# Kernel optimization log

Hardware: AMD Instinct MI355X
Metric: run time of the kernel (lower is better)

## Reference

```python
import jax, jax.numpy as jnp
import numpy as np

DIM = 1024
HEADS = 16
EPS = 1e-5  # torch nn.LayerNorm default
SCALE = (DIM / HEADS) ** -0.5


def _layernorm(x, w, b):
    mu = jnp.mean(x, axis=-1, keepdims=True)
    var = jnp.mean((x - mu) ** 2, axis=-1, keepdims=True)
    return (x - mu) * jax.lax.rsqrt(var + EPS) * w + b


def setup_inputs() -> dict:
    key = jax.random.key(0)
    ks = jax.random.split(key, 12)
    B, Lq, Lk, C, g = 2, 1024, 2048, DIM, HEADS
    c = C // g
    inp = {
        "q": jax.random.normal(ks[0], (B, Lq, C), jnp.float32),
        "k": jax.random.normal(ks[1], (B, Lk, C), jnp.float32),
        "v": jax.random.normal(ks[2], (B, Lk, C), jnp.float32),
        "qpos": jax.random.normal(ks[3], (B, Lq, g, c), jnp.float32),
        "kpos": jax.random.normal(ks[4], (B, Lk, g, c), jnp.float32),
        "mask": jax.random.randint(ks[5], (B, 1, 1, Lk), 0, 2, jnp.int32),
        # LayerNorm params
        "ln_q_w": jnp.ones((C,), jnp.float32),
        "ln_q_b": jnp.zeros((C,), jnp.float32),
        "ln_k_w": jnp.ones((C,), jnp.float32),
        "ln_k_b": jnp.zeros((C,), jnp.float32),
        "ln_v_w": jnp.ones((C,), jnp.float32),
        "ln_v_b": jnp.zeros((C,), jnp.float32),
        # Linear weights, torch layout [out, in]; qkv_bias=False
        "w_q": jax.random.normal(ks[6], (C, C), jnp.float32) * 0.02,
        "w_k": jax.random.normal(ks[7], (C, C), jnp.float32) * 0.02,
        "w_v": jax.random.normal(ks[8], (C, C), jnp.float32) * 0.02,
        "w_proj": jax.random.normal(ks[9], (C, C), jnp.float32) * 0.02,
        "b_proj": jnp.zeros((C,), jnp.float32),
    }
    return inp


def reference(q, k, v, qpos, kpos, mask,
              ln_q_w, ln_q_b, ln_k_w, ln_k_b, ln_v_w, ln_v_b,
              w_q, w_k, w_v, w_proj, b_proj):
    B, Lq, C = q.shape
    g = HEADS
    c = C // g
    Lk = k.shape[1]

    # apply_pos: pos is [B, N, g, c]; add per-head then flatten back
    q = (q.reshape(B, Lq, g, c) + qpos).reshape(B, Lq, C)
    k = (k.reshape(B, Lk, g, c) + kpos).reshape(B, Lk, C)

    qn = _layernorm(q, ln_q_w, ln_q_b)
    kn = _layernorm(k, ln_k_w, ln_k_b)
    vn = _layernorm(v, ln_v_w, ln_v_b)

    # torch Linear: x @ W.T
    q4 = jnp.einsum('bnc,dc->bnd', qn, w_q).reshape(B, Lq, g, c)
    k4 = jnp.einsum('bnc,dc->bnd', kn, w_k).reshape(B, Lk, g, c)
    v4 = jnp.einsum('bnc,dc->bnd', vn, w_v).reshape(B, Lk, g, c)

    # scores: [B, q, g, k] (note head dim is axis 2, matching original einsum)
    attn = jnp.einsum('bqgc,bkgc->bqgk', q4, k4) * SCALE
    m = mask.astype(bool)  # [B,1,1,Lk] broadcasts over q and g
    attn = jnp.where(m, -jnp.inf, attn)
    p = jax.nn.softmax(attn, axis=-1)
    p = jnp.where(m, 0.0, p)

    out = jnp.einsum('bqgk,bkgc->bqgc', p, v4).reshape(B, Lq, C)
    out = jnp.einsum('bnc,dc->bnd', out, w_proj) + b_proj
    return out
```

## Files before the change

kernel.cpp:

```cpp
#include <hip/hip_runtime.h>
#include <stdint.h>
#include <stddef.h>

typedef __bf16 bf16;
typedef bf16 bf16x2 __attribute__((ext_vector_type(2)));
typedef bf16 bf16x4 __attribute__((ext_vector_type(4)));
typedef bf16 bf16x8 __attribute__((ext_vector_type(8)));
typedef float f32x4 __attribute__((ext_vector_type(4)));
typedef float f32x16 __attribute__((ext_vector_type(16)));

#define MFMA16(a, b, c) __builtin_amdgcn_mfma_f32_16x16x32_bf16((a), (b), (c), 0, 0, 0)
#define MFMA32(a, b, c) __builtin_amdgcn_mfma_f32_32x32x16_bf16((a), (b), (c), 0, 0, 0)

#define GLD_LDS16(g, l)                                          \
    __builtin_amdgcn_global_load_lds(                            \
        (const __attribute__((address_space(1))) void*)(g),      \
        (__attribute__((address_space(3))) void*)(l), 16, 0, 0)

__global__ __launch_bounds__(256) void cast_all(const float* __restrict__ wq,
                                                const float* __restrict__ wk,
                                                const float* __restrict__ wv,
                                                const float* __restrict__ wp,
                                                bf16* __restrict__ out) {
    int i = (blockIdx.x * 256 + threadIdx.x) * 4;
    const float* src;
    int j = i;
    if (i < (1 << 20)) { src = wq; }
    else if (i < (2 << 20)) { src = wk; j = i - (1 << 20); }
    else if (i < (3 << 20)) { src = wv; j = i - (2 << 20); }
    else { src = wp; j = i - (3 << 20); }
    float4 v = *(const float4*)(src + j);
    bf16x4 o;
    o[0] = (bf16)v.x; o[1] = (bf16)v.y; o[2] = (bf16)v.z; o[3] = (bf16)v.w;
    *(bf16x4*)(out + i) = o;
}

__global__ __launch_bounds__(256) void posln_all(const float* __restrict__ q,
                                                 const float* __restrict__ k,
                                                 const float* __restrict__ v,
                                                 const float* __restrict__ qpos,
                                                 const float* __restrict__ kpos,
                                                 const float* __restrict__ lnqw,
                                                 const float* __restrict__ lnqb,
                                                 const float* __restrict__ lnkw,
                                                 const float* __restrict__ lnkb,
                                                 const float* __restrict__ lnvw,
                                                 const float* __restrict__ lnvb,
                                                 bf16* __restrict__ out) {
    int row = blockIdx.x;
    int t = threadIdx.x;
    const float *x, *pos, *w, *bb;
    int r = row;
    if (row < 2048)      { x = q; pos = qpos; w = lnqw; bb = lnqb; }
    else if (row < 6144) { r = row - 2048; x = k; pos = kpos; w = lnkw; bb = lnkb; }
    else                 { r = row - 6144; x = v; pos = nullptr; w = lnvw; bb = lnvb; }

    float4 vv = ((const float4*)(x + (size_t)r * 1024))[t];
    if (pos != nullptr) {
        float4 p = ((const float4*)(pos + (size_t)r * 1024))[t];
        vv.x += p.x; vv.y += p.y; vv.z += p.z; vv.w += p.w;
    }
    float s1 = vv.x + vv.y + vv.z + vv.w;
    float s2 = vv.x * vv.x + vv.y * vv.y + vv.z * vv.z + vv.w * vv.w;
#pragma unroll
    for (int off = 1; off < 64; off <<= 1) {
        s1 += __shfl_xor(s1, off);
        s2 += __shfl_xor(s2, off);
    }
    __shared__ float red[8];
    int wave = t >> 6;
    if ((t & 63) == 0) { red[wave * 2] = s1; red[wave * 2 + 1] = s2; }
    __syncthreads();
    s1 = red[0] + red[2] + red[4] + red[6];
    s2 = red[1] + red[3] + red[5] + red[7];
    float mu = s1 * (1.0f / 1024.0f);
    float var = s2 * (1.0f / 1024.0f) - mu * mu;
    float rstd = rsqrtf(var + 1e-5f);
    float4 wv4 = ((const float4*)w)[t];
    float4 bv4 = ((const float4*)bb)[t];
    bf16x4 o;
    o[0] = (bf16)((vv.x - mu) * rstd * wv4.x + bv4.x);
    o[1] = (bf16)((vv.y - mu) * rstd * wv4.y + bv4.y);
    o[2] = (bf16)((vv.z - mu) * rstd * wv4.z + bv4.z);
    o[3] = (bf16)((vv.w - mu) * rstd * wv4.w + bv4.w);
    *(bf16x4*)(out + (size_t)row * 1024 + t * 4) = o;
}

template <int BM, typename OutT, bool HasBias, bool VOUT>
__global__ __launch_bounds__(256) void gemm_bt(const bf16* __restrict__ A,
                                               const bf16* __restrict__ w0,
                                               const bf16* __restrict__ w1,
                                               const bf16* __restrict__ w2,
                                               int rowsW0, int rowsW01,
                                               const float* __restrict__ bias,
                                               OutT* __restrict__ out,
                                               bf16* __restrict__ vt) {
    constexpr int MF = 4;
    constexpr int NF = (BM == 128) ? 4 : 2;
    constexpr int WCSPAN = (BM == 128) ? 64 : 32;
    __shared__ bf16 As[BM * 32];
    __shared__ bf16 Bs[128 * 32];
    int bxr = blockIdx.x;
    int bx = (bxr & 7) * (gridDim.x >> 3) + (bxr >> 3);
    int tileN = bx & 7;
    int tileM = bx >> 3;
    int t = threadIdx.x;
    int wave = t >> 6, lane = t & 63;
    int lr = lane & 15, lg = lane >> 4;
    int wr = (BM == 128) ? (wave >> 1) : 0;
    int wc = (BM == 128) ? (wave & 1) : wave;
    int rowBase = tileM * BM;
    const bf16* W = (rowBase < rowsW0) ? w0 : ((rowBase < rowsW01) ? w1 : w2);
    const bf16* Ab = A + (size_t)rowBase * 1024;
    const bf16* Wb = W + (size_t)(tileN * 128) * 1024;

    int o16b0 = wave * 128 + lane;
    int o16b1 = o16b0 + 64;

    const f32x4 zero4 = {0.f, 0.f, 0.f, 0.f};
    f32x4 acc[MF][NF];
#pragma unroll
    for (int i = 0; i < MF; ++i)
#pragma unroll
        for (int j = 0; j < NF; ++j) acc[i][j] = zero4;

    for (int k0 = 0; k0 < 1024; k0 += 32) {
        if constexpr (BM == 128) {
            GLD_LDS16(Ab + (size_t)(o16b0 >> 2) * 1024 + k0 + (o16b0 & 3) * 8,
                      (char*)As + o16b0 * 16);
            GLD_LDS16(Ab + (size_t)(o16b1 >> 2) * 1024 + k0 + (o16b1 & 3) * 8,
                      (char*)As + o16b1 * 16);
        } else {
            GLD_LDS16(Ab + (size_t)(t >> 2) * 1024 + k0 + (t & 3) * 8,
                      (char*)As + t * 16);
        }
        GLD_LDS16(Wb + (size_t)(o16b0 >> 2) * 1024 + k0 + (o16b0 & 3) * 8,
                  (char*)Bs + o16b0 * 16);
        GLD_LDS16(Wb + (size_t)(o16b1 >> 2) * 1024 + k0 + (o16b1 & 3) * 8,
                  (char*)Bs + o16b1 * 16);
        __syncthreads();
        bf16x8 af[MF], bfr[NF];
#pragma unroll
        for (int mf = 0; mf < MF; ++mf)
            af[mf] = *(const bf16x8*)((const char*)As +
                                      (wr * 64 + mf * 16 + lr) * 64 + lg * 16);
#pragma unroll
        for (int nf = 0; nf < NF; ++nf)
            bfr[nf] = *(const bf16x8*)((const char*)Bs +
                                       (wc * WCSPAN + nf * 16 + lr) * 64 + lg * 16);
#pragma unroll
        for (int mf = 0; mf < MF; ++mf)
#pragma unroll
            for (int nf = 0; nf < NF; ++nf)
                acc[mf][nf] = MFMA16(af[mf], bfr[nf], acc[mf][nf]);
        __syncthreads();
    }
    bool isV = VOUT && (rowBase >= 6144);
    if (!isV) {
#pragma unroll
        for (int nf = 0; nf < NF; ++nf) {
            int ncol = tileN * 128 + wc * WCSPAN + nf * 16 + lr;
            float bv = HasBias ? bias[ncol] : 0.0f;
#pragma unroll
            for (int mf = 0; mf < MF; ++mf) {
                int mrow = rowBase + wr * 64 + mf * 16 + lg * 4;
#pragma unroll
                for (int r = 0; r < 4; ++r) {
                    float val = acc[mf][nf][r] + bv;
                    out[(size_t)(mrow + r) * 1024 + ncol] = (OutT)val;
                }
            }
        }
    } else {
        int b2 = (rowBase - 6144) >> 11;
        int kb = rowBase - 6144 - (b2 << 11);
#pragma unroll
        for (int nf = 0; nf < NF; ++nf) {
            int ncol = tileN * 128 + wc * WCSPAN + nf * 16 + lr;
            int h2 = ncol >> 6, d2 = ncol & 63;
            bf16* vrow = vt + ((size_t)((b2 * 16 + h2) * 64 + d2)) * 2048;
#pragma unroll
            for (int mf = 0; mf < MF; ++mf) {
                int kk = kb + wr * 64 + mf * 16 + lg * 4;
                bf16x4 pv;
#pragma unroll
                for (int r = 0; r < 4; ++r) pv[r] = (bf16)acc[mf][nf][r];
                *(bf16x4*)(vrow + kk) = pv;
            }
        }
    }
}

__global__ __launch_bounds__(256) void attn_kernel(const bf16* __restrict__ qkv4,
                                                   const bf16* __restrict__ vt,
                                                   const int* __restrict__ mask,
                                                   float* __restrict__ opart,
                                                   float* __restrict__ ml) {
    __shared__ float bias_s[1024];
    __shared__ bf16 Ks[2][64 * 64];
    __shared__ bf16 Vs[2][64 * 64];
    int bx = blockIdx.x;
    bx = (bx & 7) * 64 + (bx >> 3);
    int split = bx & 1, qt = (bx >> 1) & 7, h = (bx >> 4) & 15, b = bx >> 8;
    int t = threadIdx.x;
    int wave = t >> 6, lane = t & 63, lq = lane & 31, hi = lane >> 5;
    int lq7 = lq & 7;

    const int* mrow = mask + b * 2048 + split * 1024;
    for (int i = t; i < 1024; i += 256) bias_s[i] = mrow[i] ? -1e30f : 0.0f;

    int qbase = qt * 128 + wave * 32;
    const bf16* qptr = qkv4 + ((size_t)(b * 1024 + qbase + lq)) * 1024 + h * 64 + hi * 8;
    bf16x8 qf[4];
#pragma unroll
    for (int s = 0; s < 4; ++s) qf[s] = *(const bf16x8*)(qptr + s * 16);

    const bf16* kpanel = qkv4 + (size_t)(2048 + b * 2048 + split * 1024) * 1024 + h * 64;
    const bf16* vpanel = vt + ((size_t)((b * 16 + h) * 64)) * 2048 + split * 1024;

    int r0 = t >> 3, c0 = (t & 7) ^ (r0 & 7);
    int r1 = r0 + 32, c1 = (t & 7) ^ (r1 & 7);

#define STAGE(bufi, lkn)                                                      \
    {                                                                         \
        GLD_LDS16(kpanel + (size_t)((lkn) + r0) * 1024 + c0 * 8,              \
                  (char*)Ks[bufi] + t * 16);                                  \
        GLD_LDS16(kpanel + (size_t)((lkn) + r1) * 1024 + c1 * 8,              \
                  (char*)Ks[bufi] + (t + 256) * 16);                          \
        GLD_LDS16(vpanel + (size_t)r0 * 2048 + (lkn) + c0 * 8,                \
                  (char*)Vs[bufi] + t * 16);                                  \
        GLD_LDS16(vpanel + (size_t)r1 * 2048 + (lkn) + c1 * 8,                \
                  (char*)Vs[bufi] + (t + 256) * 16);                          \
    }

    f32x16 accO0 = {}, accO1 = {};
    float m_run = -1e30f, l_run = 0.0f;
    const float C_QK = 0.18033688011112042f;

#define PROCESS(bufi, s2, kloc)                                               \
    {                                                                         \
        const char* kb_ = (const char*)Ks[bufi] + ((s2) * 32 + lq) * 128;     \
        bf16x8 kf0 = *(const bf16x8*)(kb_ + (((hi + 0) ^ lq7) << 4));         \
        bf16x8 kf1 = *(const bf16x8*)(kb_ + (((hi + 2) ^ lq7) << 4));         \
        bf16x8 kf2 = *(const bf16x8*)(kb_ + (((hi + 4) ^ lq7) << 4));         \
        bf16x8 kf3 = *(const bf16x8*)(kb_ + (((hi + 6) ^ lq7) << 4));         \
        f32x16 S = {};                                                        \
        __builtin_amdgcn_s_setprio(1);                                        \
        S = MFMA32(kf0, qf[0], S);                                            \
        S = MFMA32(kf1, qf[1], S);                                            \
        S = MFMA32(kf2, qf[2], S);                                            \
        S = MFMA32(kf3, qf[3], S);                                            \
        __builtin_amdgcn_s_setprio(0);                                        \
        f32x4 bv0 = *(const f32x4*)&bias_s[(kloc) + 4 * hi];                  \
        f32x4 bv1 = *(const f32x4*)&bias_s[(kloc) + 8 + 4 * hi];              \
        f32x4 bv2 = *(const f32x4*)&bias_s[(kloc) + 16 + 4 * hi];             \
        f32x4 bv3 = *(const f32x4*)&bias_s[(kloc) + 24 + 4 * hi];             \
        float p[16];                                                          \
        float mtile = -3e38f;                                                 \
        _Pragma("unroll")                                                     \
        for (int r = 0; r < 16; ++r) {                                        \
            float bvr = (r < 4 ? bv0[r & 3] : r < 8 ? bv1[r & 3]              \
                         : r < 12 ? bv2[r & 3] : bv3[r & 3]);                 \
            p[r] = fmaf(S[r], C_QK, bvr);                                     \
            mtile = fmaxf(mtile, p[r]);                                       \
        }                                                                     \
        mtile = fmaxf(mtile, __shfl_xor(mtile, 32));                          \
        if (__any(mtile > m_run + 8.0f)) {                                    \
            float mnew = fmaxf(m_run, mtile);                                 \
            float alpha = exp2f(m_run - mnew);                                \
            m_run = mnew;                                                     \
            l_run *= alpha;                                                   \
            _Pragma("unroll")                                                 \
            for (int r = 0; r < 16; ++r) { accO0[r] *= alpha; accO1[r] *= alpha; } \
        }                                                                     \
        _Pragma("unroll")                                                     \
        for (int r = 0; r < 16; ++r) p[r] = exp2f(p[r] - m_run);              \
        float lt = ((p[0] + p[1]) + (p[2] + p[3])) + ((p[4] + p[5]) + (p[6] + p[7])) \
                 + ((p[8] + p[9]) + (p[10] + p[11])) + ((p[12] + p[13]) + (p[14] + p[15])); \
        lt += __shfl_xor(lt, 32);                                             \
        l_run += lt;                                                          \
        union { unsigned u[4]; bf16x8 v; } pf0, pf1;                          \
        _Pragma("unroll")                                                     \
        for (int w = 0; w < 4; ++w) {                                         \
            union { bf16x2 h2; unsigned u; } cv;                              \
            cv.h2[0] = (bf16)p[2 * w]; cv.h2[1] = (bf16)p[2 * w + 1];         \
            pf0.u[w] = cv.u;                                                  \
            cv.h2[0] = (bf16)p[8 + 2 * w]; cv.h2[1] = (bf16)p[9 + 2 * w];     \
            pf1.u[w] = cv.u;                                                  \
        }                                                                     \
        const char* vbA = (const char*)Vs[bufi] + lq * 128 + hi * 8;          \
        const char* vbB = vbA + 32 * 128;                                     \
        bf16x4 va[8];                                                         \
        _Pragma("unroll")                                                     \
        for (int m = 0; m < 4; ++m) {                                         \
            int cofs = ((((s2) * 4 + m) ^ lq7) << 4);                         \
            va[m] = *(const bf16x4*)(vbA + cofs);                             \
            va[4 + m] = *(const bf16x4*)(vbB + cofs);                         \
        }                                                                     \
        bf16x8 va0 = __builtin_shufflevector(va[0], va[1], 0, 1, 2, 3, 4, 5, 6, 7); \
        bf16x8 va1 = __builtin_shufflevector(va[2], va[3], 0, 1, 2, 3, 4, 5, 6, 7); \
        bf16x8 va2 = __builtin_shufflevector(va[4], va[5], 0, 1, 2, 3, 4, 5, 6, 7); \
        bf16x8 va3 = __builtin_shufflevector(va[6], va[7], 0, 1, 2, 3, 4, 5, 6, 7); \
        __builtin_amdgcn_s_setprio(1);                                        \
        accO0 = MFMA32(va0, pf0.v, accO0);                                    \
        accO0 = MFMA32(va1, pf1.v, accO0);                                    \
        accO1 = MFMA32(va2, pf0.v, accO1);                                    \
        accO1 = MFMA32(va3, pf1.v, accO1);                                    \
        __builtin_amdgcn_s_setprio(0);                                        \
    }

    STAGE(0, 0);
    __syncthreads();
    int buf = 0;
    for (int it = 0; it < 16; ++it) {
        if (it < 15) STAGE(buf ^ 1, (it + 1) * 64);
        PROCESS(buf, 0, it * 64);
        PROCESS(buf, 1, it * 64 + 32);
        __syncthreads();
        buf ^= 1;
    }
#undef STAGE
#undef PROCESS

    size_t orow = (size_t)(split * 2048 + b * 1024 + qbase + lq);
    float* op = opart + orow * 1024 + h * 64;
#pragma unroll
    for (int m = 0; m < 4; ++m) {
        float4 v0 = {accO0[4 * m], accO0[4 * m + 1], accO0[4 * m + 2], accO0[4 * m + 3]};
        *(float4*)(op + 8 * m + 4 * hi) = v0;
        float4 v1 = {accO1[4 * m], accO1[4 * m + 1], accO1[4 * m + 2], accO1[4 * m + 3]};
        *(float4*)(op + 32 + 8 * m + 4 * hi) = v1;
    }
    if (lane < 32) {
        float2 mlv = {m_run, l_run};
        *(float2*)(ml + (orow * 16 + h) * 2) = mlv;
    }
}

__global__ __launch_bounds__(256) void combine_kernel(const float* __restrict__ opart,
                                                      const float* __restrict__ ml,
                                                      bf16* __restrict__ out) {
    int row = blockIdx.x;
    int t = threadIdx.x;
    int h = t >> 4;
    const float* ml0 = ml + ((size_t)row * 16 + h) * 2;
    const float* ml1 = ml + ((size_t)(2048 + row) * 16 + h) * 2;
    float m0 = ml0[0], l0 = ml0[1], m1 = ml1[0], l1 = ml1[1];
    float ms = fmaxf(m0, m1);
    float w0 = exp2f(m0 - ms), w1 = exp2f(m1 - ms);
    float inv = 1.0f / (w0 * l0 + w1 * l1);
    f32x4 o0 = *(const f32x4*)(opart + (size_t)row * 1024 + t * 4);
    f32x4 o1 = *(const f32x4*)(opart + (size_t)(2048 + row) * 1024 + t * 4);
    bf16x4 r;
#pragma unroll
    for (int c = 0; c < 4; ++c) r[c] = (bf16)((o0[c] * w0 + o1[c] * w1) * inv);
    *(bf16x4*)(out + (size_t)row * 1024 + t * 4) = r;
}

extern "C" void kernel_launch(void* const* d_in, const int* in_sizes, int n_in,
                              void* d_out, int out_size, void* d_ws, size_t ws_size,
                              hipStream_t stream) {
    const float* q    = (const float*)d_in[0];
    const float* k    = (const float*)d_in[1];
    const float* v    = (const float*)d_in[2];
    const float* qpos = (const float*)d_in[3];
    const float* kpos = (const float*)d_in[4];
    const int*   mask = (const int*)d_in[5];
    const float* lnqw = (const float*)d_in[6];
    const float* lnqb = (const float*)d_in[7];
    const float* lnkw = (const float*)d_in[8];
    const float* lnkb = (const float*)d_in[9];
    const float* lnvw = (const float*)d_in[10];
    const float* lnvb = (const float*)d_in[11];
    const float* wq   = (const float*)d_in[12];
    const float* wk   = (const float*)d_in[13];
    const float* wv   = (const float*)d_in[14];
    const float* wp   = (const float*)d_in[15];
    const float* bp   = (const float*)d_in[16];
    float* out = (float*)d_out;

    char* ws = (char*)d_ws;
    const size_t MB = 1024 * 1024;
    bf16*  wq_b  = (bf16*)(ws + 0 * MB);
    bf16*  wk_b  = (bf16*)(ws + 2 * MB);
    bf16*  wv_b  = (bf16*)(ws + 4 * MB);
    bf16*  wp_b  = (bf16*)(ws + 6 * MB);
    bf16*  xn    = (bf16*)(ws + 8 * MB);
    float* opart = (float*)(ws + 8 * MB);
    float* mlbuf = (float*)(ws + 24 * MB);
    bf16*  qkv4  = (bf16*)(ws + 28 * MB);
    bf16*  vtb   = (bf16*)(ws + 40 * MB);
    bf16*  attn  = (bf16*)(ws + 0 * MB);

    cast_all<<<4096, 256, 0, stream>>>(wq, wk, wv, wp, wq_b);

    posln_all<<<10240, 256, 0, stream>>>(q, k, v, qpos, kpos,
                                         lnqw, lnqb, lnkw, lnkb, lnvw, lnvb, xn);

    gemm_bt<128, bf16, false, true><<<640, 256, 0, stream>>>(
        xn, wq_b, wk_b, wv_b, 2048, 6144, nullptr, qkv4, vtb);

    attn_kernel<<<512, 256, 0, stream>>>(qkv4, vtb, mask, opart, mlbuf);

    combine_kernel<<<2048, 256, 0, stream>>>(opart, mlbuf, attn);

    gemm_bt<64, float, true, false><<<256, 256, 0, stream>>>(
        attn, wp_b, wp_b, wp_b, 1 << 20, 1 << 20, bp, out, nullptr);
}
```

Before: 123.2 us.

## Split attention KV into four chunks and store normalized bf16 partials

Splits the key/value sequence four ways instead of two, doubling the attention grid to 1024 blocks to better fill the CUs. Each block normalizes its partial output by its own row sum and writes it as bf16 instead of fp32, which halves partial-output traffic. The combine kernel now merges four partials weighted by exp2(m-M)*l. The added bf16 rounding of partials costs some precision, and the shorter per-block loop gives fewer iterations to amortize setup and pipeline fill.

```diff
diff --git a/kernel.cpp b/kernel.cpp
--- a/kernel.cpp
+++ b/kernel.cpp
@@ -194,20 +194,20 @@
 __global__ __launch_bounds__(256) void attn_kernel(const bf16* __restrict__ qkv4,
                                                    const bf16* __restrict__ vt,
                                                    const int* __restrict__ mask,
-                                                   float* __restrict__ opart,
+                                                   bf16* __restrict__ opart,
                                                    float* __restrict__ ml) {
-    __shared__ float bias_s[1024];
+    __shared__ float bias_s[512];
     __shared__ bf16 Ks[2][64 * 64];
     __shared__ bf16 Vs[2][64 * 64];
     int bx = blockIdx.x;
-    bx = (bx & 7) * 64 + (bx >> 3);
-    int split = bx & 1, qt = (bx >> 1) & 7, h = (bx >> 4) & 15, b = bx >> 8;
+    bx = (bx & 7) * 128 + (bx >> 3);
+    int split = bx & 3, qt = (bx >> 2) & 7, h = (bx >> 5) & 15, b = bx >> 9;
     int t = threadIdx.x;
     int wave = t >> 6, lane = t & 63, lq = lane & 31, hi = lane >> 5;
     int lq7 = lq & 7;
 
-    const int* mrow = mask + b * 2048 + split * 1024;
-    for (int i = t; i < 1024; i += 256) bias_s[i] = mrow[i] ? -1e30f : 0.0f;
+    const int* mrow = mask + b * 2048 + split * 512;
+    for (int i = t; i < 512; i += 256) bias_s[i] = mrow[i] ? -1e30f : 0.0f;
 
     int qbase = qt * 128 + wave * 32;
     const bf16* qptr = qkv4 + ((size_t)(b * 1024 + qbase + lq)) * 1024 + h * 64 + hi * 8;
@@ -215,8 +215,8 @@
 #pragma unroll
     for (int s = 0; s < 4; ++s) qf[s] = *(const bf16x8*)(qptr + s * 16);
 
-    const bf16* kpanel = qkv4 + (size_t)(2048 + b * 2048 + split * 1024) * 1024 + h * 64;
-    const bf16* vpanel = vt + ((size_t)((b * 16 + h) * 64)) * 2048 + split * 1024;
+    const bf16* kpanel = qkv4 + (size_t)(2048 + b * 2048 + split * 512) * 1024 + h * 64;
+    const bf16* vpanel = vt + ((size_t)((b * 16 + h) * 64)) * 2048 + split * 512;
 
     int r0 = t >> 3, c0 = (t & 7) ^ (r0 & 7);
     int r1 = r0 + 32, c1 = (t & 7) ^ (r1 & 7);
@@ -312,8 +312,8 @@
     STAGE(0, 0);
     __syncthreads();
     int buf = 0;
-    for (int it = 0; it < 16; ++it) {
-        if (it < 15) STAGE(buf ^ 1, (it + 1) * 64);
+    for (int it = 0; it < 8; ++it) {
+        if (it < 7) STAGE(buf ^ 1, (it + 1) * 64);
         PROCESS(buf, 0, it * 64);
         PROCESS(buf, 1, it * 64 + 32);
         __syncthreads();
@@ -322,14 +322,19 @@
 #undef STAGE
 #undef PROCESS
 
+    float linv = (l_run > 0.0f) ? (1.0f / l_run) : 0.0f;
     size_t orow = (size_t)(split * 2048 + b * 1024 + qbase + lq);
-    float* op = opart + orow * 1024 + h * 64;
+    bf16* op = opart + orow * 1024 + h * 64;
 #pragma unroll
     for (int m = 0; m < 4; ++m) {
-        float4 v0 = {accO0[4 * m], accO0[4 * m + 1], accO0[4 * m + 2], accO0[4 * m + 3]};
-        *(float4*)(op + 8 * m + 4 * hi) = v0;
-        float4 v1 = {accO1[4 * m], accO1[4 * m + 1], accO1[4 * m + 2], accO1[4 * m + 3]};
-        *(float4*)(op + 32 + 8 * m + 4 * hi) = v1;
+        bf16x4 y0, y1;
+#pragma unroll
+        for (int r = 0; r < 4; ++r) {
+            y0[r] = (bf16)(accO0[4 * m + r] * linv);
+            y1[r] = (bf16)(accO1[4 * m + r] * linv);
+        }
+        *(bf16x4*)(op + 8 * m + 4 * hi) = y0;
+        *(bf16x4*)(op + 32 + 8 * m + 4 * hi) = y1;
     }
     if (lane < 32) {
         float2 mlv = {m_run, l_run};
@@ -337,23 +342,33 @@
     }
 }
 
-__global__ __launch_bounds__(256) void combine_kernel(const float* __restrict__ opart,
+__global__ __launch_bounds__(256) void combine_kernel(const bf16* __restrict__ opart,
                                                       const float* __restrict__ ml,
                                                       bf16* __restrict__ out) {
     int row = blockIdx.x;
     int t = threadIdx.x;
     int h = t >> 4;
-    const float* ml0 = ml + ((size_t)row * 16 + h) * 2;
-    const float* ml1 = ml + ((size_t)(2048 + row) * 16 + h) * 2;
-    float m0 = ml0[0], l0 = ml0[1], m1 = ml1[0], l1 = ml1[1];
-    float ms = fmaxf(m0, m1);
-    float w0 = exp2f(m0 - ms), w1 = exp2f(m1 - ms);
-    float inv = 1.0f / (w0 * l0 + w1 * l1);
-    f32x4 o0 = *(const f32x4*)(opart + (size_t)row * 1024 + t * 4);
-    f32x4 o1 = *(const f32x4*)(opart + (size_t)(2048 + row) * 1024 + t * 4);
+    float m[4], l[4];
+#pragma unroll
+    for (int s = 0; s < 4; ++s) {
+        const float* p = ml + ((size_t)(s * 2048 + row) * 16 + h) * 2;
+        m[s] = p[0]; l[s] = p[1];
+    }
+    float M = fmaxf(fmaxf(m[0], m[1]), fmaxf(m[2], m[3]));
+    float u[4], denom = 0.0f;
+#pragma unroll
+    for (int s = 0; s < 4; ++s) { u[s] = exp2f(m[s] - M) * l[s]; denom += u[s]; }
+    float inv = (denom > 0.0f) ? (1.0f / denom) : 0.0f;
+    float acc[4] = {0.f, 0.f, 0.f, 0.f};
+#pragma unroll
+    for (int s = 0; s < 4; ++s) {
+        bf16x4 y = *(const bf16x4*)(opart + (size_t)(s * 2048 + row) * 1024 + t * 4);
+#pragma unroll
+        for (int c = 0; c < 4; ++c) acc[c] += u[s] * (float)y[c];
+    }
     bf16x4 r;
 #pragma unroll
-    for (int c = 0; c < 4; ++c) r[c] = (bf16)((o0[c] * w0 + o1[c] * w1) * inv);
+    for (int c = 0; c < 4; ++c) r[c] = (bf16)(acc[c] * inv);
     *(bf16x4*)(out + (size_t)row * 1024 + t * 4) = r;
 }
 
@@ -386,7 +401,7 @@
     bf16*  wv_b  = (bf16*)(ws + 4 * MB);
     bf16*  wp_b  = (bf16*)(ws + 6 * MB);
     bf16*  xn    = (bf16*)(ws + 8 * MB);
-    float* opart = (float*)(ws + 8 * MB);
+    bf16*  opart = (bf16*)(ws + 8 * MB);
     float* mlbuf = (float*)(ws + 24 * MB);
     bf16*  qkv4  = (bf16*)(ws + 28 * MB);
     bf16*  vtb   = (bf16*)(ws + 40 * MB);
@@ -400,7 +415,7 @@
     gemm_bt<128, bf16, false, true><<<640, 256, 0, stream>>>(
         xn, wq_b, wk_b, wv_b, 2048, 6144, nullptr, qkv4, vtb);
 
-    attn_kernel<<<512, 256, 0, stream>>>(qkv4, vtb, mask, opart, mlbuf);
+    attn_kernel<<<1024, 256, 0, stream>>>(qkv4, vtb, mask, opart, mlbuf);
 
     combine_kernel<<<2048, 256, 0, stream>>>(opart, mlbuf, attn);
 
```

After: 122.5 us. About the same (-0.6%).
